# Kernel optimization log

Measured on AMD Instinct MI355X. Metric: run time of the kernel, lower is better.

The kernel has to match this reference:

```python
import jax, jax.numpy as jnp
import numpy as np


def setup_inputs() -> dict:
    key = jax.random.key(0)
    k1, k2, k3 = jax.random.split(key, 3)
    B, C, H, W = 512, 4, 125, 125
    img = jax.random.normal(k1, (B, C, H, W), dtype=jnp.float32)
    # fc: Linear(62500 -> 20), Tanh, Dropout(eval=identity), Linear(20 -> 1), Sigmoid
    W1 = jax.random.normal(k2, (C * H * W, 20), dtype=jnp.float32) * 0.004  # ~1/sqrt(62500)
    b1 = jnp.zeros((20,), dtype=jnp.float32)
    W2 = jax.random.normal(k3, (20, 1), dtype=jnp.float32) * 0.2
    b2 = jnpp = jnp.zeros((1,), dtype=jnp.float32)
    return {"img": img, "W1": W1, "b1": b1, "W2": W2, "b2": b2}


def reference(img, W1, b1, W2, b2):
    B, C, H, W = img.shape
    # small MLP -> rotation angle theta in [0, 2*pi)
    h = jnp.tanh(img.reshape(B, -1) @ W1 + b1)          # (B, 20)
    theta = jax.nn.sigmoid(h @ W2 + b2)[:, 0] * (2.0 * np.pi)  # (B,)
    c, s = jnp.cos(theta), jnp.sin(theta)
    z = jnp.zeros_like(c)
    # (B, 2, 3) affine matrix: pure rotation, zero translation
    Mat = jnp.stack([jnp.stack([c, -s, z], axis=-1),
                     jnp.stack([s,  c, z], axis=-1)], axis=-2)

    # affine_grid, align_corners=True: normalized coords span [-1, 1] at pixel centers
    ys = jnp.linspace(-1.0, 1.0, H, dtype=img.dtype)
    xs = jnp.linspace(-1.0, 1.0, W, dtype=img.dtype)
    gy, gx = jnp.meshgrid(ys, xs, indexing="ij")        # (H, W)
    base = jnp.stack([gx, gy, jnp.ones_like(gx)], axis=-1)  # (H, W, 3) homogeneous (x, y, 1)
    grid = jnp.einsum("bij,hwj->bhwi", Mat, base)       # (B, H, W, 2) -> (x, y)

    # grid_sample: bilinear, padding_mode='zeros', align_corners=True
    ix = (grid[..., 0] + 1.0) * 0.5 * (W - 1)
    iy = (grid[..., 1] + 1.0) * 0.5 * (H - 1)
    ix0 = jnp.floor(ix); iy0 = jnp.floor(iy)
    ix1 = ix0 + 1.0;     iy1 = iy0 + 1.0
    wx1 = ix - ix0; wx0 = 1.0 - wx1
    wy1 = iy - iy0; wy0 = 1.0 - wy1

    def gather(ixi, iyi):
        valid = (ixi >= 0) & (ixi <= W - 1) & (iyi >= 0) & (iyi <= H - 1)
        xc = jnp.clip(ixi, 0, W - 1).astype(jnp.int32)
        yc = jnp.clip(iyi, 0, H - 1).astype(jnp.int32)
        vals = jax.vmap(lambda im, yy, xx: im[:, yy, xx])(img, yc, xc)  # (B, C, H, W)
        return vals * valid[:, None, :, :].astype(img.dtype)

    out = (gather(ix0, iy0) * (wx0 * wy0)[:, None]
         + gather(ix1, iy0) * (wx1 * wy0)[:, None]
         + gather(ix0, iy1) * (wx0 * wy1)[:, None]
         + gather(ix1, iy1) * (wx1 * wy1)[:, None])
    return out, Mat
```

## Files before the change

### kernel.cpp

```cpp
#include <hip/hip_runtime.h>
#include <hip/hip_bf16.h>
#include <math.h>

#define K_TOT 62500
#define KQ_TOT 15625
#define NJ    20
#define NB    512
#define HW_   15625
#define WW_   125
#define NKSPL 128
#define LDSTR 68
#define SWSTR 124

#define HP_OFF   0
#define HRED_OFF (NKSPL * NJ * NB)
#define W1T_OFF  2000000
#define MAT_OFF  32000000

__global__ __launch_bounds__(256) void k0_transpose(const float* __restrict__ W1,
                                                    float* __restrict__ W1T) {
    const int k = blockIdx.x * 256 + threadIdx.x;
    if (k >= K_TOT) return;
    const float* src = W1 + (size_t)k * NJ;
#pragma unroll
    for (int j = 0; j < NJ; ++j)
        W1T[(size_t)j * K_TOT + k] = src[j];
}

__global__ __launch_bounds__(256, 2) void k1_partial(const float* __restrict__ img,
                                                     const float* __restrict__ W1T,
                                                     float* __restrict__ hpart) {
    __shared__ float  simg[2][64 * LDSTR];
    __shared__ float4 sw[NJ * SWSTR];
    const int tid  = threadIdx.x;
    const int bx   = blockIdx.x;
    const int b0   = blockIdx.y << 6;
    const int lane = tid & 63;
    const int j0   = __builtin_amdgcn_readfirstlane((tid >> 6) * 5);
    const int srow = tid >> 4;
    const int squad = tid & 15;

    const int q0  = (bx * KQ_TOT) >> 7;
    const int q1  = ((bx + 1) * KQ_TOT) >> 7;
    const int nqb = q1 - q0;
    const int nsteps = (nqb + 15) >> 4;

    const float4* img4 = reinterpret_cast<const float4*>(img);
    const float4* W1T4 = reinterpret_cast<const float4*>(W1T);

    for (int i = tid; i < NJ * 128; i += 256) {
        const int j  = i >> 7;
        const int qq = i & 127;
        if (qq < nqb)
            sw[j * SWSTR + qq] = W1T4[(size_t)j * KQ_TOT + q0 + qq];
    }

    float acc0 = 0.f, acc1 = 0.f, acc2 = 0.f, acc3 = 0.f, acc4 = 0.f;

    {
        const int cq = (nqb < 16) ? nqb : 16;
        if (squad < cq) {
            const int qg = q0 + squad;
#pragma unroll
            for (int rr = 0; rr < 4; ++rr) {
                const int row = srow + (rr << 4);
                *reinterpret_cast<float4*>(&simg[0][row * LDSTR + (squad << 2)]) =
                    img4[(size_t)(b0 + row) * KQ_TOT + qg];
            }
        }
    }
    __syncthreads();

    int cur = 0;
    for (int s = 0; s < nsteps; ++s) {
        float4 r0, r1, r2, r3;
        bool dl = false;
        if (s + 1 < nsteps) {
            const int rem = nqb - (s + 1) * 16;
            const int cq  = (rem < 16) ? rem : 16;
            if (squad < cq) {
                dl = true;
                const size_t qg = (size_t)q0 + (s + 1) * 16 + squad;
                r0 = img4[(size_t)(b0 + srow +  0) * KQ_TOT + qg];
                r1 = img4[(size_t)(b0 + srow + 16) * KQ_TOT + qg];
                r2 = img4[(size_t)(b0 + srow + 32) * KQ_TOT + qg];
                r3 = img4[(size_t)(b0 + srow + 48) * KQ_TOT + qg];
            }
        }

        {
            const int rem = nqb - s * 16;
            const int cq  = (rem < 16) ? rem : 16;
            const float* simgl = &simg[cur][lane * LDSTR];
            const int qbase = s * 16;
#pragma unroll 4
            for (int q = 0; q < cq; ++q) {
                const float4 iv = *reinterpret_cast<const float4*>(&simgl[q << 2]);
                const int qi = qbase + q;
                const float4 w0 = sw[(j0 + 0) * SWSTR + qi];
                const float4 w1 = sw[(j0 + 1) * SWSTR + qi];
                const float4 w2 = sw[(j0 + 2) * SWSTR + qi];
                const float4 w3 = sw[(j0 + 3) * SWSTR + qi];
                const float4 w4 = sw[(j0 + 4) * SWSTR + qi];
                acc0 += iv.x * w0.x + iv.y * w0.y + iv.z * w0.z + iv.w * w0.w;
                acc1 += iv.x * w1.x + iv.y * w1.y + iv.z * w1.z + iv.w * w1.w;
                acc2 += iv.x * w2.x + iv.y * w2.y + iv.z * w2.z + iv.w * w2.w;
                acc3 += iv.x * w3.x + iv.y * w3.y + iv.z * w3.z + iv.w * w3.w;
                acc4 += iv.x * w4.x + iv.y * w4.y + iv.z * w4.z + iv.w * w4.w;
            }
        }

        if (dl) {
            float* d = &simg[cur ^ 1][srow * LDSTR + (squad << 2)];
            *reinterpret_cast<float4*>(&d[ 0 * LDSTR]) = r0;
            *reinterpret_cast<float4*>(&d[16 * LDSTR]) = r1;
            *reinterpret_cast<float4*>(&d[32 * LDSTR]) = r2;
            *reinterpret_cast<float4*>(&d[48 * LDSTR]) = r3;
        }
        __syncthreads();
        cur ^= 1;
    }

    const int b = b0 + lane;
    float* dst = &hpart[(size_t)(bx * NJ + j0) * NB + b];
    dst[0 * NB] = acc0;
    dst[1 * NB] = acc1;
    dst[2 * NB] = acc2;
    dst[3 * NB] = acc3;
    dst[4 * NB] = acc4;
}

__global__ __launch_bounds__(256) void k2_reduce(const float* __restrict__ hpart,
                                                 float* __restrict__ hred) {
    const int b = blockIdx.x * 256 + threadIdx.x;
    const int j = blockIdx.y;
    float a = 0.f;
#pragma unroll 8
    for (int c = 0; c < NKSPL; ++c)
        a += hpart[(size_t)(c * NJ + j) * NB + b];
    hred[j * NB + b] = a;
}

__global__ __launch_bounds__(256) void k2_head(const float* __restrict__ hred,
                                               const float* __restrict__ b1,
                                               const float* __restrict__ W2,
                                               const float* __restrict__ b2,
                                               float* __restrict__ mat) {
    const int b = blockIdx.x * 256 + threadIdx.x;
    float z = b2[0];
#pragma unroll
    for (int j = 0; j < NJ; ++j) {
        const float h = tanhf(hred[j * NB + b] + b1[j]);
        z += h * W2[j];
    }
    const float sg = 1.0f / (1.0f + expf(-z));
    const float theta = sg * 6.28318530717958647692f;
    float sn, cn;
    sincosf(theta, &sn, &cn);
    float* m = mat + (size_t)b * 6;
    m[0] = cn; m[1] = -sn; m[2] = 0.f;
    m[3] = sn; m[4] = cn;  m[5] = 0.f;
}

__device__ __forceinline__ unsigned int pack2bf(float a, float b) {
    __hip_bfloat16 ha = __float2bfloat16(a);
    __hip_bfloat16 hb = __float2bfloat16(b);
    const unsigned int ua = (unsigned int)__builtin_bit_cast(unsigned short, ha);
    const unsigned int ub = (unsigned int)__builtin_bit_cast(unsigned short, hb);
    return ua | (ub << 16);
}
#define BF_LO(u) __uint_as_float((u) << 16)
#define BF_HI(u) __uint_as_float((u) & 0xffff0000u)

__global__ __launch_bounds__(1024) void k3_sample(const float* __restrict__ img,
                                                  const float* __restrict__ mat,
                                                  float* __restrict__ out) {
    __shared__ unsigned int sch[HW_];
    const int b   = blockIdx.x;
    const int tid = threadIdx.x;

    const float cb = mat[(size_t)b * 6 + 4];
    const float sb = mat[(size_t)b * 6 + 3];
    const size_t ib = (size_t)b * 4 * HW_;

#pragma unroll
    for (int pair = 0; pair < 2; ++pair) {
        const float* pa = img + ib + (size_t)(2 * pair) * HW_;
        const float* pb = pa + HW_;
        __syncthreads();
        for (int i = tid; i < HW_; i += 1024)
            sch[i] = pack2bf(pa[i], pb[i]);
        __syncthreads();

        float* oa = out + ib + (size_t)(2 * pair) * HW_;
        for (int p = tid; p < HW_; p += 1024) {
            const int y = p / WW_;
            const int x = p - y * WW_;

            const float gx = (float)x * (1.0f / 62.0f) - 1.0f;
            const float gy = (float)y * (1.0f / 62.0f) - 1.0f;
            const float fx = (cb * gx - sb * gy + 1.0f) * 62.0f;
            const float fy = (sb * gx + cb * gy + 1.0f) * 62.0f;

            const float x0f = floorf(fx), y0f = floorf(fy);
            const int x0 = (int)x0f, y0 = (int)y0f;
            const int x1 = x0 + 1, y1 = y0 + 1;
            const float wx1 = fx - x0f, wx0 = 1.0f - wx1;
            const float wy1 = fy - y0f, wy0 = 1.0f - wy1;

            const bool vx0 = ((unsigned)x0 <= 124u);
            const bool vx1 = ((unsigned)x1 <= 124u);
            const bool vy0 = ((unsigned)y0 <= 124u);
            const bool vy1 = ((unsigned)y1 <= 124u);

            const int cx0 = min(max(x0, 0), 124), cx1 = min(max(x1, 0), 124);
            const int cy0 = min(max(y0, 0), 124), cy1 = min(max(y1, 0), 124);

            const float m00 = (vx0 && vy0) ? wx0 * wy0 : 0.f;
            const float m01 = (vx1 && vy0) ? wx1 * wy0 : 0.f;
            const float m10 = (vx0 && vy1) ? wx0 * wy1 : 0.f;
            const float m11 = (vx1 && vy1) ? wx1 * wy1 : 0.f;

            const unsigned int q00 = sch[cy0 * WW_ + cx0];
            const unsigned int q01 = sch[cy0 * WW_ + cx1];
            const unsigned int q10 = sch[cy1 * WW_ + cx0];
            const unsigned int q11 = sch[cy1 * WW_ + cx1];

            float a0, a1;
            a0  = BF_LO(q00) * m00;  a1  = BF_HI(q00) * m00;
            a0 += BF_LO(q01) * m01;  a1 += BF_HI(q01) * m01;
            a0 += BF_LO(q10) * m10;  a1 += BF_HI(q10) * m10;
            a0 += BF_LO(q11) * m11;  a1 += BF_HI(q11) * m11;

            oa[p]       = a0;
            oa[p + HW_] = a1;
        }
    }
}

extern "C" void kernel_launch(void* const* d_in, const int* in_sizes, int n_in,
                              void* d_out, int out_size, void* d_ws, size_t ws_size,
                              hipStream_t stream) {
    const float* img = (const float*)d_in[0];
    const float* W1  = (const float*)d_in[1];
    const float* b1  = (const float*)d_in[2];
    const float* W2  = (const float*)d_in[3];
    const float* b2  = (const float*)d_in[4];
    float* out = (float*)d_out;

    float* hpart = out + HP_OFF;
    float* hred  = out + HRED_OFF;
    float* W1T   = out + W1T_OFF;
    float* mat   = out + MAT_OFF;

    hipLaunchKernelGGL(k0_transpose, dim3((K_TOT + 255) / 256), dim3(256), 0, stream, W1, W1T);
    hipLaunchKernelGGL(k1_partial, dim3(NKSPL, 8), dim3(256), 0, stream, img, W1T, hpart);
    hipLaunchKernelGGL(k2_reduce, dim3(2, NJ), dim3(256), 0, stream, hpart, hred);
    hipLaunchKernelGGL(k2_head, dim3(2), dim3(256), 0, stream, hred, b1, W2, b2, mat);
    hipLaunchKernelGGL(k3_sample, dim3(NB), dim3(1024), 0, stream, img, mat, out);
}
```

Before: 125.3 us.

## Read W1 from global in matvec, fuse reduce into head, sample four channels per pass

The partial-matvec kernel stops staging W1T slices in LDS and reads the weights straight from global memory with wave-uniform addresses. It also raises the occupancy hint to 3 and fully unrolls the full 16-quad steps. The separate reduce kernel is folded into the head kernel, which now sums all 128 partials itself in only 2 blocks, so one launch goes away but that reduction becomes far less parallel. The sampler packs all four channels as bf16 into one uint2 LDS array and processes them in a single pass, removing one fill and a barrier at the cost of 125 KB of LDS per block.

```diff
diff --git a/kernel.cpp b/kernel.cpp
--- a/kernel.cpp
+++ b/kernel.cpp
@@ -10,10 +10,8 @@
 #define WW_   125
 #define NKSPL 128
 #define LDSTR 68
-#define SWSTR 124
 
 #define HP_OFF   0
-#define HRED_OFF (NKSPL * NJ * NB)
 #define W1T_OFF  2000000
 #define MAT_OFF  32000000
 
@@ -27,11 +25,10 @@
         W1T[(size_t)j * K_TOT + k] = src[j];
 }
 
-__global__ __launch_bounds__(256, 2) void k1_partial(const float* __restrict__ img,
+__global__ __launch_bounds__(256, 3) void k1_partial(const float* __restrict__ img,
                                                      const float* __restrict__ W1T,
                                                      float* __restrict__ hpart) {
-    __shared__ float  simg[2][64 * LDSTR];
-    __shared__ float4 sw[NJ * SWSTR];
+    __shared__ float simg[2][64 * LDSTR];
     const int tid  = threadIdx.x;
     const int bx   = blockIdx.x;
     const int b0   = blockIdx.y << 6;
@@ -40,33 +37,28 @@
     const int srow = tid >> 4;
     const int squad = tid & 15;
 
-    const int q0  = (bx * KQ_TOT) >> 7;
-    const int q1  = ((bx + 1) * KQ_TOT) >> 7;
+    const int q0  = (int)(((long long)bx * KQ_TOT) >> 7);
+    const int q1  = (int)(((long long)(bx + 1) * KQ_TOT) >> 7);
     const int nqb = q1 - q0;
     const int nsteps = (nqb + 15) >> 4;
 
     const float4* img4 = reinterpret_cast<const float4*>(img);
     const float4* W1T4 = reinterpret_cast<const float4*>(W1T);
-
-    for (int i = tid; i < NJ * 128; i += 256) {
-        const int j  = i >> 7;
-        const int qq = i & 127;
-        if (qq < nqb)
-            sw[j * SWSTR + qq] = W1T4[(size_t)j * KQ_TOT + q0 + qq];
-    }
+    const float4* wj0 = W1T4 + (size_t)(j0 + 0) * KQ_TOT;
+    const float4* wj1 = W1T4 + (size_t)(j0 + 1) * KQ_TOT;
+    const float4* wj2 = W1T4 + (size_t)(j0 + 2) * KQ_TOT;
+    const float4* wj3 = W1T4 + (size_t)(j0 + 3) * KQ_TOT;
+    const float4* wj4 = W1T4 + (size_t)(j0 + 4) * KQ_TOT;
 
     float acc0 = 0.f, acc1 = 0.f, acc2 = 0.f, acc3 = 0.f, acc4 = 0.f;
 
     {
-        const int cq = (nqb < 16) ? nqb : 16;
-        if (squad < cq) {
-            const int qg = q0 + squad;
-#pragma unroll
-            for (int rr = 0; rr < 4; ++rr) {
-                const int row = srow + (rr << 4);
-                *reinterpret_cast<float4*>(&simg[0][row * LDSTR + (squad << 2)]) =
-                    img4[(size_t)(b0 + row) * KQ_TOT + qg];
-            }
+        const int qg = q0 + squad;
+#pragma unroll
+        for (int rr = 0; rr < 4; ++rr) {
+            const int row = srow + (rr << 4);
+            *reinterpret_cast<float4*>(&simg[0][row * LDSTR + (squad << 2)]) =
+                img4[(size_t)(b0 + row) * KQ_TOT + qg];
         }
     }
     __syncthreads();
@@ -90,23 +82,39 @@
 
         {
             const int rem = nqb - s * 16;
-            const int cq  = (rem < 16) ? rem : 16;
             const float* simgl = &simg[cur][lane * LDSTR];
-            const int qbase = s * 16;
-#pragma unroll 4
-            for (int q = 0; q < cq; ++q) {
-                const float4 iv = *reinterpret_cast<const float4*>(&simgl[q << 2]);
-                const int qi = qbase + q;
-                const float4 w0 = sw[(j0 + 0) * SWSTR + qi];
-                const float4 w1 = sw[(j0 + 1) * SWSTR + qi];
-                const float4 w2 = sw[(j0 + 2) * SWSTR + qi];
-                const float4 w3 = sw[(j0 + 3) * SWSTR + qi];
-                const float4 w4 = sw[(j0 + 4) * SWSTR + qi];
-                acc0 += iv.x * w0.x + iv.y * w0.y + iv.z * w0.z + iv.w * w0.w;
-                acc1 += iv.x * w1.x + iv.y * w1.y + iv.z * w1.z + iv.w * w1.w;
-                acc2 += iv.x * w2.x + iv.y * w2.y + iv.z * w2.z + iv.w * w2.w;
-                acc3 += iv.x * w3.x + iv.y * w3.y + iv.z * w3.z + iv.w * w3.w;
-                acc4 += iv.x * w4.x + iv.y * w4.y + iv.z * w4.z + iv.w * w4.w;
+            const int qb = q0 + s * 16;
+            if (rem >= 16) {
+#pragma unroll
+                for (int q = 0; q < 16; ++q) {
+                    const float4 iv = *reinterpret_cast<const float4*>(&simgl[q << 2]);
+                    const int qi = qb + q;
+                    const float4 w0 = wj0[qi];
+                    const float4 w1 = wj1[qi];
+                    const float4 w2 = wj2[qi];
+                    const float4 w3 = wj3[qi];
+                    const float4 w4 = wj4[qi];
+                    acc0 += iv.x * w0.x + iv.y * w0.y + iv.z * w0.z + iv.w * w0.w;
+                    acc1 += iv.x * w1.x + iv.y * w1.y + iv.z * w1.z + iv.w * w1.w;
+                    acc2 += iv.x * w2.x + iv.y * w2.y + iv.z * w2.z + iv.w * w2.w;
+                    acc3 += iv.x * w3.x + iv.y * w3.y + iv.z * w3.z + iv.w * w3.w;
+                    acc4 += iv.x * w4.x + iv.y * w4.y + iv.z * w4.z + iv.w * w4.w;
+                }
+            } else {
+                for (int q = 0; q < rem; ++q) {
+                    const float4 iv = *reinterpret_cast<const float4*>(&simgl[q << 2]);
+                    const int qi = qb + q;
+                    const float4 w0 = wj0[qi];
+                    const float4 w1 = wj1[qi];
+                    const float4 w2 = wj2[qi];
+                    const float4 w3 = wj3[qi];
+                    const float4 w4 = wj4[qi];
+                    acc0 += iv.x * w0.x + iv.y * w0.y + iv.z * w0.z + iv.w * w0.w;
+                    acc1 += iv.x * w1.x + iv.y * w1.y + iv.z * w1.z + iv.w * w1.w;
+                    acc2 += iv.x * w2.x + iv.y * w2.y + iv.z * w2.z + iv.w * w2.w;
+                    acc3 += iv.x * w3.x + iv.y * w3.y + iv.z * w3.z + iv.w * w3.w;
+                    acc4 += iv.x * w4.x + iv.y * w4.y + iv.z * w4.z + iv.w * w4.w;
+                }
             }
         }
 
@@ -130,18 +138,7 @@
     dst[4 * NB] = acc4;
 }
 
-__global__ __launch_bounds__(256) void k2_reduce(const float* __restrict__ hpart,
-                                                 float* __restrict__ hred) {
-    const int b = blockIdx.x * 256 + threadIdx.x;
-    const int j = blockIdx.y;
-    float a = 0.f;
-#pragma unroll 8
-    for (int c = 0; c < NKSPL; ++c)
-        a += hpart[(size_t)(c * NJ + j) * NB + b];
-    hred[j * NB + b] = a;
-}
-
-__global__ __launch_bounds__(256) void k2_head(const float* __restrict__ hred,
+__global__ __launch_bounds__(256) void k2_head(const float* __restrict__ hpart,
                                                const float* __restrict__ b1,
                                                const float* __restrict__ W2,
                                                const float* __restrict__ b2,
@@ -150,7 +147,11 @@
     float z = b2[0];
 #pragma unroll
     for (int j = 0; j < NJ; ++j) {
-        const float h = tanhf(hred[j * NB + b] + b1[j]);
+        float a = 0.f;
+#pragma unroll 8
+        for (int c = 0; c < NKSPL; ++c)
+            a += hpart[(size_t)(c * NJ + j) * NB + b];
+        const float h = tanhf(a + b1[j]);
         z += h * W2[j];
     }
     const float sg = 1.0f / (1.0f + expf(-z));
@@ -175,66 +176,74 @@
 __global__ __launch_bounds__(1024) void k3_sample(const float* __restrict__ img,
                                                   const float* __restrict__ mat,
                                                   float* __restrict__ out) {
-    __shared__ unsigned int sch[HW_];
+    __shared__ uint2 sch[HW_];
     const int b   = blockIdx.x;
     const int tid = threadIdx.x;
 
     const float cb = mat[(size_t)b * 6 + 4];
     const float sb = mat[(size_t)b * 6 + 3];
     const size_t ib = (size_t)b * 4 * HW_;
-
-#pragma unroll
-    for (int pair = 0; pair < 2; ++pair) {
-        const float* pa = img + ib + (size_t)(2 * pair) * HW_;
-        const float* pb = pa + HW_;
-        __syncthreads();
-        for (int i = tid; i < HW_; i += 1024)
-            sch[i] = pack2bf(pa[i], pb[i]);
-        __syncthreads();
-
-        float* oa = out + ib + (size_t)(2 * pair) * HW_;
-        for (int p = tid; p < HW_; p += 1024) {
-            const int y = p / WW_;
-            const int x = p - y * WW_;
-
-            const float gx = (float)x * (1.0f / 62.0f) - 1.0f;
-            const float gy = (float)y * (1.0f / 62.0f) - 1.0f;
-            const float fx = (cb * gx - sb * gy + 1.0f) * 62.0f;
-            const float fy = (sb * gx + cb * gy + 1.0f) * 62.0f;
-
-            const float x0f = floorf(fx), y0f = floorf(fy);
-            const int x0 = (int)x0f, y0 = (int)y0f;
-            const int x1 = x0 + 1, y1 = y0 + 1;
-            const float wx1 = fx - x0f, wx0 = 1.0f - wx1;
-            const float wy1 = fy - y0f, wy0 = 1.0f - wy1;
-
-            const bool vx0 = ((unsigned)x0 <= 124u);
-            const bool vx1 = ((unsigned)x1 <= 124u);
-            const bool vy0 = ((unsigned)y0 <= 124u);
-            const bool vy1 = ((unsigned)y1 <= 124u);
-
-            const int cx0 = min(max(x0, 0), 124), cx1 = min(max(x1, 0), 124);
-            const int cy0 = min(max(y0, 0), 124), cy1 = min(max(y1, 0), 124);
-
-            const float m00 = (vx0 && vy0) ? wx0 * wy0 : 0.f;
-            const float m01 = (vx1 && vy0) ? wx1 * wy0 : 0.f;
-            const float m10 = (vx0 && vy1) ? wx0 * wy1 : 0.f;
-            const float m11 = (vx1 && vy1) ? wx1 * wy1 : 0.f;
-
-            const unsigned int q00 = sch[cy0 * WW_ + cx0];
-            const unsigned int q01 = sch[cy0 * WW_ + cx1];
-            const unsigned int q10 = sch[cy1 * WW_ + cx0];
-            const unsigned int q11 = sch[cy1 * WW_ + cx1];
-
-            float a0, a1;
-            a0  = BF_LO(q00) * m00;  a1  = BF_HI(q00) * m00;
-            a0 += BF_LO(q01) * m01;  a1 += BF_HI(q01) * m01;
-            a0 += BF_LO(q10) * m10;  a1 += BF_HI(q10) * m10;
-            a0 += BF_LO(q11) * m11;  a1 += BF_HI(q11) * m11;
-
-            oa[p]       = a0;
-            oa[p + HW_] = a1;
-        }
+    const float* p0 = img + ib;
+    const float* p1 = p0 + HW_;
+    const float* p2 = p1 + HW_;
+    const float* p3 = p2 + HW_;
+
+    for (int i = tid; i < HW_; i += 1024) {
+        uint2 q;
+        q.x = pack2bf(p0[i], p1[i]);
+        q.y = pack2bf(p2[i], p3[i]);
+        sch[i] = q;
+    }
+    __syncthreads();
+
+    float* o0 = out + ib;
+    for (int p = tid; p < HW_; p += 1024) {
+        const int y = p / WW_;
+        const int x = p - y * WW_;
+
+        const float gx = (float)x * (1.0f / 62.0f) - 1.0f;
+        const float gy = (float)y * (1.0f / 62.0f) - 1.0f;
+        const float fx = (cb * gx - sb * gy + 1.0f) * 62.0f;
+        const float fy = (sb * gx + cb * gy + 1.0f) * 62.0f;
+
+        const float x0f = floorf(fx), y0f = floorf(fy);
+        const int x0 = (int)x0f, y0 = (int)y0f;
+        const int x1 = x0 + 1, y1 = y0 + 1;
+        const float wx1 = fx - x0f, wx0 = 1.0f - wx1;
+        const float wy1 = fy - y0f, wy0 = 1.0f - wy1;
+
+        const bool vx0 = ((unsigned)x0 <= 124u);
+        const bool vx1 = ((unsigned)x1 <= 124u);
+        const bool vy0 = ((unsigned)y0 <= 124u);
+        const bool vy1 = ((unsigned)y1 <= 124u);
+
+        const int cx0 = min(max(x0, 0), 124), cx1 = min(max(x1, 0), 124);
+        const int cy0 = min(max(y0, 0), 124), cy1 = min(max(y1, 0), 124);
+
+        const float m00 = (vx0 && vy0) ? wx0 * wy0 : 0.f;
+        const float m01 = (vx1 && vy0) ? wx1 * wy0 : 0.f;
+        const float m10 = (vx0 && vy1) ? wx0 * wy1 : 0.f;
+        const float m11 = (vx1 && vy1) ? wx1 * wy1 : 0.f;
+
+        const uint2 q00 = sch[cy0 * WW_ + cx0];
+        const uint2 q01 = sch[cy0 * WW_ + cx1];
+        const uint2 q10 = sch[cy1 * WW_ + cx0];
+        const uint2 q11 = sch[cy1 * WW_ + cx1];
+
+        float a0, a1, a2, a3;
+        a0  = BF_LO(q00.x) * m00;  a1  = BF_HI(q00.x) * m00;
+        a2  = BF_LO(q00.y) * m00;  a3  = BF_HI(q00.y) * m00;
+        a0 += BF_LO(q01.x) * m01;  a1 += BF_HI(q01.x) * m01;
+        a2 += BF_LO(q01.y) * m01;  a3 += BF_HI(q01.y) * m01;
+        a0 += BF_LO(q10.x) * m10;  a1 += BF_HI(q10.x) * m10;
+        a2 += BF_LO(q10.y) * m10;  a3 += BF_HI(q10.y) * m10;
+        a0 += BF_LO(q11.x) * m11;  a1 += BF_HI(q11.x) * m11;
+        a2 += BF_LO(q11.y) * m11;  a3 += BF_HI(q11.y) * m11;
+
+        o0[p]            = a0;
+        o0[p + 1 * HW_]  = a1;
+        o0[p + 2 * HW_]  = a2;
+        o0[p + 3 * HW_]  = a3;
     }
 }
 
@@ -249,13 +258,11 @@
     float* out = (float*)d_out;
 
     float* hpart = out + HP_OFF;
-    float* hred  = out + HRED_OFF;
     float* W1T   = out + W1T_OFF;
     float* mat   = out + MAT_OFF;
 
     hipLaunchKernelGGL(k0_transpose, dim3((K_TOT + 255) / 256), dim3(256), 0, stream, W1, W1T);
     hipLaunchKernelGGL(k1_partial, dim3(NKSPL, 8), dim3(256), 0, stream, img, W1T, hpart);
-    hipLaunchKernelGGL(k2_reduce, dim3(2, NJ), dim3(256), 0, stream, hpart, hred);
-    hipLaunchKernelGGL(k2_head, dim3(2), dim3(256), 0, stream, hred, b1, W2, b2, mat);
+    hipLaunchKernelGGL(k2_head, dim3(2), dim3(256), 0, stream, hpart, b1, W2, b2, mat);
     hipLaunchKernelGGL(k3_sample, dim3(NB), dim3(1024), 0, stream, img, mat, out);
 }
```

Measured after the change: 290.5 us. 2.32x slower.
